# Kernel tuning notes

Measured on AMD Instinct MI355X. Metric: run time of the kernel, lower is better.

## Reference

```python
import jax, jax.numpy as jnp
import numpy as np

B, L, S, STATIC = 32, 512, 37, 8
D, DI, N, K, DTR, NL, V = 768, 1536, 16, 4, 48, 4, 32


def _rmsnorm(h, w, eps=1e-5):
    var = jnp.mean(h * h, axis=-1, keepdims=True)
    return h * jax.lax.rsqrt(var + eps) * w


def _layernorm(h, w, b, eps=1e-5):
    mu = jnp.mean(h, axis=-1, keepdims=True)
    var = jnp.mean((h - mu) ** 2, axis=-1, keepdims=True)
    return (h - mu) * jax.lax.rsqrt(var + eps) * w + b


def _selective_scan(u, dt, A, Bm, Cm):
    # u, dt: [B,L,Di]; A: [Di,N]; Bm, Cm: [B,L,N]
    def step(h, inp):
        u_t, dt_t, B_t, C_t = inp              # [B,Di],[B,Di],[B,N],[B,N]
        dA = jnp.exp(dt_t[..., None] * A)      # [B,Di,N]
        h = dA * h + (dt_t * u_t)[..., None] * B_t[:, None, :]
        y = jnp.einsum('bdn,bn->bd', h, C_t)
        return h, y
    h0 = jnp.zeros((u.shape[0], DI, N), u.dtype)
    xs = (u.transpose(1, 0, 2), dt.transpose(1, 0, 2),
          Bm.transpose(1, 0, 2), Cm.transpose(1, 0, 2))
    _, ys = jax.lax.scan(step, h0, xs)
    return ys.transpose(1, 0, 2)  # [B,L,Di]


def setup_inputs() -> dict:
    key = jax.random.key(0)
    ks = jax.random.split(key, 24)
    s = 0.02
    inp = {
        'x': jax.random.normal(ks[0], (B, L, S), jnp.float32),
        'static': jax.random.normal(ks[1], (B, STATIC), jnp.float32),
        'time': jax.random.uniform(ks[2], (B, L), jnp.float32),
        'sensor_mask': jax.random.randint(ks[3], (B, L, S), 0, 2, jnp.int32),
        'labels': jax.random.randint(ks[4], (B, L), 0, V, jnp.int64),
        # CEHR embedding params
        'emb_w': jax.random.normal(ks[5], (D, 2 * S), jnp.float32) * s,
        'emb_b': jnp.zeros((D,), jnp.float32),
        'static_w': jax.random.normal(ks[6], (D, STATIC), jnp.float32) * s,
        'static_b': jnp.zeros((D,), jnp.float32),
        'ln_w': jnp.ones((D,), jnp.float32),
        'ln_b': jnp.zeros((D,), jnp.float32),
        # Mamba layers (stacked)
        'norm_w': jnp.ones((NL, D), jnp.float32),
        'in_proj_w': jax.random.normal(ks[7], (NL, 2 * DI, D), jnp.float32) * s,
        'conv_w': jax.random.normal(ks[8], (NL, DI, K), jnp.float32) * s,
        'conv_b': jnp.zeros((NL, DI), jnp.float32),
        'x_proj_w': jax.random.normal(ks[9], (NL, DTR + 2 * N, DI), jnp.float32) * s,
        'dt_proj_w': jax.random.normal(ks[10], (NL, DI, DTR), jnp.float32) * s,
        'dt_proj_b': jnp.full((NL, DI), -4.6, jnp.float32),  # softplus^-1(~0.01)
        'A_log': jnp.broadcast_to(jnp.log(jnp.arange(1, N + 1, dtype=jnp.float32)), (NL, DI, N)).copy(),
        'D_param': jnp.ones((NL, DI), jnp.float32),
        'out_proj_w': jax.random.normal(ks[11], (NL, D, DI), jnp.float32) * s,
        'norm_f_w': jnp.ones((D,), jnp.float32),
        'lm_head_w': jax.random.normal(ks[12], (V, D), jnp.float32) * s,
    }
    return inp


def reference(x, static, time, sensor_mask, labels, emb_w, emb_b, static_w,
              static_b, ln_w, ln_b, norm_w, in_proj_w, conv_w, conv_b,
              x_proj_w, dt_proj_w, dt_proj_b, A_log, D_param, out_proj_w,
              norm_f_w, lm_head_w):
    # ---- CEHR embedding: concat(values, mask) -> D, plus static broadcast ----
    feats = jnp.concatenate([x, sensor_mask.astype(x.dtype)], axis=-1)  # [B,L,2S]
    h = jnp.einsum('blf,df->bld', feats, emb_w) + emb_b
    h = h + (static @ static_w.T + static_b)[:, None, :]
    h = _layernorm(h, ln_w, ln_b)  # [B,L,D]

    # ---- Mamba backbone ----
    for l in range(NL):
        resid = h
        hn = _rmsnorm(h, norm_w[l])
        xz = jnp.einsum('bld,ed->ble', hn, in_proj_w[l])  # [B,L,2*Di]
        xb, z = jnp.split(xz, 2, axis=-1)
        # causal depthwise conv1d, kernel K
        xp = jnp.pad(xb, ((0, 0), (K - 1, 0), (0, 0)))
        xc = sum(conv_w[l][:, k] * xp[:, k:k + L, :] for k in range(K)) + conv_b[l]
        xc = jax.nn.silu(xc)
        proj = jnp.einsum('bld,ed->ble', xc, x_proj_w[l])  # [B,L,DTR+2N]
        dt_r = proj[..., :DTR]
        Bm = proj[..., DTR:DTR + N]
        Cm = proj[..., DTR + N:]
        dt = jax.nn.softplus(jnp.einsum('blr,dr->bld', dt_r, dt_proj_w[l]) + dt_proj_b[l])
        A = -jnp.exp(A_log[l])  # [Di,N]
        y = _selective_scan(xc, dt, A, Bm, Cm) + D_param[l] * xc
        y = y * jax.nn.silu(z)
        h = resid + jnp.einsum('ble,de->bld', y, out_proj_w[l])

    h = _rmsnorm(h, norm_f_w)
    logits = jnp.einsum('bld,vd->blv', h, lm_head_w)  # [B,L,V]
    return logits
```

## Files before the change

kernel.cpp:

```cpp
#include <hip/hip_runtime.h>
#include <math.h>

#define B_ 32
#define L_ 512
#define S_ 37
#define STATIC_ 8
#define D_ 768
#define DI_ 1536
#define N_ 16
#define DTR_ 48
#define NL_ 4
#define V_ 32
#define ROWS_ (B_*L_)
#define KE_ 96
#define TCH_ 64
#define NCHT_ (L_/TCH_)
#define KS_ 4
#define KSL_ (DI_/KS_)
#define TPW_ 66
#define TPO_ 68

typedef __bf16 bf16;
typedef __bf16 bf16x8 __attribute__((ext_vector_type(8)));
typedef __bf16 bf16x4 __attribute__((ext_vector_type(4)));
typedef __bf16 bf16x2 __attribute__((ext_vector_type(2)));
typedef float f32x4 __attribute__((ext_vector_type(4)));

typedef __attribute__((address_space(3))) void lds_void;
typedef __attribute__((address_space(1))) const void gmem_void;

__device__ __forceinline__ void gld16(const void* g, void* l) {
    __builtin_amdgcn_global_load_lds((gmem_void*)g, (lds_void*)l, 16, 0, 0);
}

__device__ __forceinline__ float silu_(float x) { return x / (1.f + __expf(-x)); }
__device__ __forceinline__ float softplus_(float x) {
    return fmaxf(x, 0.f) + __logf(1.f + __expf(-fabsf(x)));
}
__device__ __forceinline__ unsigned pack_bf2_(float a, float b) {
    bf16x2 v{(bf16)a, (bf16)b};
    return __builtin_bit_cast(unsigned, v);
}
template<int CTRL>
__device__ __forceinline__ float dpp_add_(float p) {
    int vi = __builtin_amdgcn_update_dpp(0, __builtin_bit_cast(int, p),
                                         CTRL, 0xF, 0xF, true);
    return p + __builtin_bit_cast(float, vi);
}

template<int MODE>
__global__ __launch_bounds__(256) void gemm_mfma(
    const bf16* __restrict__ A, const bf16* __restrict__ W,
    const float* __restrict__ addsrc, void* __restrict__ Cv,
    int Nstore, int K, int ntn,
    const float* __restrict__ dt_bias, unsigned* __restrict__ swg,
    float* __restrict__ pbuf, const bf16* __restrict__ uref)
{
    __shared__ bf16 As[128 * 32];
    __shared__ bf16 Bs[128 * 32];
    const int tid = threadIdx.x;

    int m0, n0, kbeg, kend;
    if (MODE == 4) {
        m0 = blockIdx.y * 128; n0 = 0;
        kbeg = blockIdx.x * KSL_; kend = kbeg + KSL_;
    } else {
        int bid = blockIdx.x;
        int xcd = bid & 7, slot = bid >> 3;
        int Mtiles = gridDim.x / ntn;
        int mband = Mtiles >> 3;
        int m_tile = xcd * mband + slot / ntn;
        int n_tile = slot % ntn;
        m0 = m_tile * 128; n0 = n_tile * 128;
        kbeg = 0; kend = K;
    }

    f32x4 acc[4][4];
    #pragma unroll
    for (int i = 0; i < 4; i++)
        #pragma unroll
        for (int j = 0; j < 4; j++)
            acc[i][j] = f32x4{0.f, 0.f, 0.f, 0.f};

    const int srow = tid >> 2, spart = tid & 3;
    const bf16* ag = A + (size_t)(m0 + srow) * K + spart * 8;
    const bf16* wg = W + (size_t)(n0 + srow) * K + spart * 8;
    char* lA = (char*)As + tid * 16;
    char* lB = (char*)Bs + tid * 16;

    const int lane = tid & 63, wv = tid >> 6;
    const int wr = wv >> 1, wc = wv & 1;
    const int colL = lane & 15, quad = lane >> 4;
    const bf16* aRd = As + (wr * 64 + colL) * 32 + quad * 8;
    const bf16* bRd = Bs + (wc * 64 + colL) * 32 + quad * 8;

    for (int kt = kbeg; kt < kend; kt += 32) {
        gld16(ag + kt, lA);
        gld16(ag + kt + (size_t)64 * K, lA + 4096);
        gld16(wg + kt, lB);
        gld16(wg + kt + (size_t)64 * K, lB + 4096);
        __syncthreads();
        bf16x8 fa[4], fb[4];
        #pragma unroll
        for (int i = 0; i < 4; i++) fa[i] = *(const bf16x8*)(aRd + i * 16 * 32);
        #pragma unroll
        for (int j = 0; j < 4; j++) fb[j] = *(const bf16x8*)(bRd + j * 16 * 32);
        #pragma unroll
        for (int i = 0; i < 4; i++)
            #pragma unroll
            for (int j = 0; j < 4; j++)
                acc[i][j] = __builtin_amdgcn_mfma_f32_16x16x32_bf16(fa[i], fb[j], acc[i][j], 0, 0, 0);
        __syncthreads();
    }

    float* Cf = (float*)Cv;
    bf16*  Cb = (bf16*)Cv;
    #pragma unroll
    for (int i = 0; i < 4; i++) {
        #pragma unroll
        for (int j = 0; j < 4; j++) {
            int n = n0 + wc * 64 + j * 16 + colL;
            #pragma unroll
            for (int r = 0; r < 4; r++) {
                int m = m0 + wr * 64 + i * 16 + quad * 4 + r;
                float v = acc[i][j][r];
                if (MODE == 2) {
                    float dtv = softplus_(v + dt_bias[n]);
                    float u = (float)uref[(size_t)m * DI_ + n];
                    swg[(size_t)m * DI_ + n] = pack_bf2_(dtv * u, dtv);
                } else if (MODE == 4) {
                    if (n < 96)
                        pbuf[((size_t)blockIdx.x * Nstore + m) * 96 + n] = v;
                } else if (n < Nstore) {
                    if (addsrc) v += addsrc[(size_t)m * Nstore + n];
                    if (MODE == 1) Cb[(size_t)m * Nstore + n] = (bf16)v;
                    else           Cf[(size_t)m * Nstore + n] = v;
                }
            }
        }
    }
}

template<int MODE>
__global__ __launch_bounds__(512, 2) void gemm256(
    const bf16* __restrict__ A, const bf16* __restrict__ W,
    const float* __restrict__ addsrc, void* __restrict__ Cv,
    int Nstore, int K, int ntn)
{
    __shared__ bf16 lds[65536];
    const int tid = threadIdx.x;

    const int bid = blockIdx.x;
    const int qx = gridDim.x >> 3;
    const int wgid = (bid & 7) * qx + (bid >> 3);
    const int m0 = (wgid / ntn) * 256;
    const int n0 = (wgid % ntn) * 256;

    const int r0 = tid >> 3;
    const int scol = ((tid & 7) * 8) ^ ((r0 & 7) << 3);
    const size_t sK = (size_t)K;
    const bf16* aSrc = A + (size_t)(m0 + r0) * sK + scol;
    const bf16* bSrc = W + (size_t)(n0 + r0) * sK + scol;
    char* ldst = (char*)lds + tid * 16;

#define STAGE_A(h, t) { const bf16* s_ = aSrc + (size_t)(h) * 128 * sK + (t) * 64;   \
    char* d_ = ldst + ((t) & 1) * 65536 + (h) * 16384;                               \
    gld16(s_, d_); gld16(s_ + 64 * sK, d_ + 8192); }
#define STAGE_B(h, t) { const bf16* s_ = bSrc + (size_t)(h) * 128 * sK + (t) * 64;   \
    char* d_ = ldst + ((t) & 1) * 65536 + 32768 + (h) * 16384;                       \
    gld16(s_, d_); gld16(s_ + 64 * sK, d_ + 8192); }

    const int lane = tid & 63, w = tid >> 6;
    const int wr = w >> 2, wc = w & 3;
    const int colL = lane & 15, quad = lane >> 4;
    const int sx = (colL & 7) << 3;
    const int c0 = (quad * 8) ^ sx;
    const int c1 = c0 ^ 32;
    const bf16* aRd0 = lds + wr * 8192 + colL * 64 + c0;
    const bf16* aRd1 = lds + wr * 8192 + colL * 64 + c1;
    const bf16* bRd0 = lds + 16384 + (wc >> 1) * 8192 + ((wc & 1) * 64 + colL) * 64 + c0;
    const bf16* bRd1 = lds + 16384 + (wc >> 1) * 8192 + ((wc & 1) * 64 + colL) * 64 + c1;

    f32x4 acc[8][4];
    #pragma unroll
    for (int i = 0; i < 8; i++)
        #pragma unroll
        for (int j = 0; j < 4; j++)
            acc[i][j] = f32x4{0.f, 0.f, 0.f, 0.f};
    bf16x8 aF[4][2], bF[4][2];

#define RD_A(buf, mp) { _Pragma("unroll") for (int i = 0; i < 4; i++) {              \
    aF[i][0] = *(const bf16x8*)(aRd0 + (buf) * 32768 + (mp) * 4096 + i * 1024);      \
    aF[i][1] = *(const bf16x8*)(aRd1 + (buf) * 32768 + (mp) * 4096 + i * 1024); } }
#define RD_B01(buf) { _Pragma("unroll") for (int j = 0; j < 2; j++) {                \
    bF[j][0] = *(const bf16x8*)(bRd0 + (buf) * 32768 + j * 1024);                    \
    bF[j][1] = *(const bf16x8*)(bRd1 + (buf) * 32768 + j * 1024); } }
#define RD_B23(buf) { _Pragma("unroll") for (int j = 0; j < 2; j++) {                \
    bF[2 + j][0] = *(const bf16x8*)(bRd0 + (buf) * 32768 + (2 + j) * 1024);          \
    bF[2 + j][1] = *(const bf16x8*)(bRd1 + (buf) * 32768 + (2 + j) * 1024); } }
#define MM(mp, np) { _Pragma("unroll") for (int i = 0; i < 4; i++)                   \
    _Pragma("unroll") for (int j = 0; j < 2; j++) {                                  \
    acc[(mp)*4+i][(np)*2+j] = __builtin_amdgcn_mfma_f32_16x16x32_bf16(               \
        aF[i][0], bF[(np)*2+j][0], acc[(mp)*4+i][(np)*2+j], 0, 0, 0);                \
    acc[(mp)*4+i][(np)*2+j] = __builtin_amdgcn_mfma_f32_16x16x32_bf16(               \
        aF[i][1], bF[(np)*2+j][1], acc[(mp)*4+i][(np)*2+j], 0, 0, 0); } }
#define MID_SYNC  __builtin_amdgcn_s_barrier();                                      \
    asm volatile("s_waitcnt lgkmcnt(0)" ::: "memory");                               \
    __builtin_amdgcn_sched_barrier(0);                                               \
    __builtin_amdgcn_s_setprio(1);
#define END_PHASE __builtin_amdgcn_s_setprio(0); __builtin_amdgcn_s_barrier();

    const int NT = K >> 6;
    const int NI = NT >> 1;

    STAGE_B(0, 0); STAGE_B(1, 0); STAGE_A(0, 0); STAGE_A(1, 0);
    STAGE_B(0, 1); STAGE_B(1, 1);
    asm volatile("s_waitcnt vmcnt(4)" ::: "memory");
    __builtin_amdgcn_s_barrier();

    for (int it = 0; it < NI; ++it) {
        const int t0 = 2 * it, t1 = t0 + 1;
        const bool nlast = (it + 1 < NI);
        RD_A(0, 0); RD_B01(0);
        STAGE_A(0, t1);
        MID_SYNC; MM(0, 0); END_PHASE;
        RD_B23(0);
        STAGE_A(1, t1);
        MID_SYNC; MM(0, 1); END_PHASE;
        RD_A(0, 1);
        if (nlast) STAGE_B(0, t0 + 2);
        MID_SYNC; MM(1, 0); END_PHASE;
        if (nlast) STAGE_B(1, t0 + 2);
        MID_SYNC; MM(1, 1);
        __builtin_amdgcn_s_setprio(0);
        if (nlast) { asm volatile("s_waitcnt vmcnt(4)" ::: "memory"); }
        else       { asm volatile("s_waitcnt vmcnt(0)" ::: "memory"); }
        __builtin_amdgcn_s_barrier();
        RD_A(1, 0); RD_B01(1);
        if (nlast) STAGE_A(0, t0 + 2);
        MID_SYNC; MM(0, 0); END_PHASE;
        RD_B23(1);
        if (nlast) STAGE_A(1, t0 + 2);
        MID_SYNC; MM(0, 1); END_PHASE;
        RD_A(1, 1);
        if (nlast) STAGE_B(0, t1 + 2);
        MID_SYNC; MM(1, 0); END_PHASE;
        if (nlast) STAGE_B(1, t1 + 2);
        MID_SYNC; MM(1, 1);
        __builtin_amdgcn_s_setprio(0);
        if (nlast) { asm volatile("s_waitcnt vmcnt(4)" ::: "memory"); }
        __builtin_amdgcn_s_barrier();
    }

    float* Cf = (float*)Cv;
    bf16*  Cb = (bf16*)Cv;
    #pragma unroll
    for (int f = 0; f < 8; f++) {
        #pragma unroll
        for (int j = 0; j < 4; j++) {
            int n = n0 + wc * 64 + j * 16 + colL;
            #pragma unroll
            for (int r = 0; r < 4; r++) {
                int m = m0 + wr * 128 + f * 16 + quad * 4 + r;
                float v = acc[f][j][r];
                if (MODE == 0) {
                    v += addsrc[(size_t)m * Nstore + n];
                    Cf[(size_t)m * Nstore + n] = v;
                } else {
                    Cb[(size_t)m * Nstore + n] = (bf16)v;
                }
            }
        }
    }
#undef STAGE_A
#undef STAGE_B
#undef RD_A
#undef RD_B01
#undef RD_B23
#undef MM
#undef MID_SYNC
#undef END_PHASE
}

__global__ __launch_bounds__(256) void xpost_kernel(const float* __restrict__ pbuf,
                                                    bf16* __restrict__ dtr,
                                                    float* __restrict__ bcf,
                                                    int crows) {
    int idx = blockIdx.x * 256 + threadIdx.x;
    int m = idx / 96, j = idx % 96;
    float s = pbuf[idx];
    #pragma unroll
    for (int k = 1; k < KS_; k++) s += pbuf[(size_t)k * crows * 96 + idx];
    if (j < 64) {
        dtr[(size_t)m * 64 + j] = (bf16)s;
    } else {
        int jj = j - 64;
        int n = jj & 15, hi = jj >> 4;
        int bb = m >> 9, t = m & 511;
        int ct = t >> 6, tl = t & 63;
        int byo = (n * 512 + tl * 8 + hi * 4) ^ ((n & 7) << 4);
        *(float*)((char*)bcf + (size_t)(bb * 8 + ct) * 8192 + byo) = s;
    }
}

__global__ __launch_bounds__(256) void cast_f2b_kernel(const float* __restrict__ s,
                                                       bf16* __restrict__ d) {
    size_t i = (size_t)blockIdx.x * 256 + threadIdx.x;
    d[i] = (bf16)s[i];
}

__global__ __launch_bounds__(256) void pad_lm_kernel(const float* __restrict__ s, bf16* __restrict__ d) {
    int i = blockIdx.x * 256 + threadIdx.x;
    int row = i / D_;
    d[i] = (row < V_) ? (bf16)s[i] : (bf16)0.f;
}

__global__ __launch_bounds__(256) void pad_embw_kernel(const float* __restrict__ s, bf16* __restrict__ d) {
    int i = blockIdx.x * 256 + threadIdx.x;
    int row = i / KE_, col = i % KE_;
    d[i] = (col < 2 * S_) ? (bf16)s[row * 2 * S_ + col] : (bf16)0.f;
}

__global__ __launch_bounds__(256) void feats_kernel(const float* __restrict__ x,
                                                    const int* __restrict__ mask,
                                                    bf16* __restrict__ d) {
    size_t i = (size_t)blockIdx.x * 256 + threadIdx.x;
    size_t row = i / KE_;
    int col = (int)(i % KE_);
    float v = 0.f;
    if (col < S_) v = x[row * S_ + col];
    else if (col < 2 * S_) v = (float)mask[row * S_ + (col - S_)];
    d[i] = (bf16)v;
}

__global__ __launch_bounds__(256) void xpw_pad_kernel(const float* __restrict__ xpw,
                                                      bf16* __restrict__ d) {
    int l = blockIdx.y;
    int idx = blockIdx.x * 256 + threadIdx.x;
    int row = idx / DI_, col = idx % DI_;
    float v = 0.f;
    if (row < DTR_) v = xpw[((size_t)l * (DTR_ + 2 * N_) + row) * DI_ + col];
    else if (row >= 64 && row < 96) v = xpw[((size_t)l * (DTR_ + 2 * N_) + row - 16) * DI_ + col];
    d[(size_t)l * 128 * DI_ + idx] = (bf16)v;
}

__global__ __launch_bounds__(256) void dtw_pad_kernel(const float* __restrict__ dtw,
                                                      bf16* __restrict__ d) {
    int l = blockIdx.y;
    int idx = blockIdx.x * 256 + threadIdx.x;
    int row = idx / 64, c = idx % 64;
    float v = (c < DTR_) ? dtw[((size_t)l * DI_ + row) * DTR_ + c] : 0.f;
    d[(size_t)l * DI_ * 64 + idx] = (bf16)v;
}

__global__ __launch_bounds__(256) void sstat_kernel(const float* __restrict__ stat,
                                                    const float* __restrict__ static_w,
                                                    const float* __restrict__ static_b,
                                                    const float* __restrict__ emb_b,
                                                    float* __restrict__ sstat) {
    int i = blockIdx.x * 256 + threadIdx.x;
    int d = i % D_, b = i / D_;
    float acc = emb_b[d] + static_b[d];
    const float* sw = static_w + (size_t)d * STATIC_;
    const float* sv = stat + (size_t)b * STATIC_;
    #pragma unroll
    for (int s = 0; s < STATIC_; s++) acc += sv[s] * sw[s];
    sstat[i] = acc;
}

__device__ __forceinline__ void block_reduce2_(float& a, float& b, float* sbuf) {
    #pragma unroll
    for (int off = 32; off > 0; off >>= 1) {
        a += __shfl_down(a, off, 64);
        b += __shfl_down(b, off, 64);
    }
    int lane = threadIdx.x & 63, wid = threadIdx.x >> 6;
    if (lane == 0) { sbuf[wid] = a; sbuf[4 + wid] = b; }
    __syncthreads();
    a = sbuf[0] + sbuf[1] + sbuf[2] + sbuf[3];
    b = sbuf[4] + sbuf[5] + sbuf[6] + sbuf[7];
}

__global__ __launch_bounds__(256) void ln_embed_kernel(const float* __restrict__ h_pre,
                                                       const float* __restrict__ sstat,
                                                       const float* __restrict__ ln_w,
                                                       const float* __restrict__ ln_b,
                                                       float* __restrict__ h) {
    int row = blockIdx.x, b = row / L_, tid = threadIdx.x;
    __shared__ float sbuf[8];
    float v[3], sum = 0.f, sq = 0.f;
    #pragma unroll
    for (int j = 0; j < 3; j++) {
        int d = tid + 256 * j;
        v[j] = h_pre[(size_t)row * D_ + d] + sstat[b * D_ + d];
        sum += v[j]; sq += v[j] * v[j];
    }
    block_reduce2_(sum, sq, sbuf);
    float mu = sum * (1.f / D_);
    float rstd = rsqrtf(sq * (1.f / D_) - mu * mu + 1e-5f);
    #pragma unroll
    for (int j = 0; j < 3; j++) {
        int d = tid + 256 * j;
        h[(size_t)row * D_ + d] = (v[j] - mu) * rstd * ln_w[d] + ln_b[d];
    }
}

__global__ __launch_bounds__(256) void rmsnorm_bf_kernel(const float* __restrict__ h,
                                                         const float* __restrict__ w,
                                                         bf16* __restrict__ out) {
    int row = blockIdx.x, tid = threadIdx.x;
    __shared__ float sbuf[8];
    float v[3], ss = 0.f, dummy = 0.f;
    #pragma unroll
    for (int j = 0; j < 3; j++) {
        v[j] = h[(size_t)row * D_ + tid + 256 * j];
        ss += v[j] * v[j];
    }
    block_reduce2_(ss, dummy, sbuf);
    float rstd = rsqrtf(ss * (1.f / D_) + 1e-5f);
    #pragma unroll
    for (int j = 0; j < 3; j++) {
        int d = tid + 256 * j;
        out[(size_t)row * D_ + d] = (bf16)(v[j] * rstd * w[d]);
    }
}

__global__ __launch_bounds__(256) void conv_silu_kernel(const bf16* __restrict__ xzb,
                                                        const float* __restrict__ cw,
                                                        const float* __restrict__ cb,
                                                        const float* __restrict__ Dp,
                                                        bf16* __restrict__ xcb,
                                                        unsigned* __restrict__ gag) {
    size_t idx = (size_t)blockIdx.x * 256 + threadIdx.x;
    int d4 = (int)(idx % (DI_ / 4));
    size_t row = idx / (DI_ / 4);
    int t = (int)(row % L_);
    int d = d4 * 4;
    const uint2* xz64 = (const uint2*)xzb;
    size_t base = row * 768 + d4;
    uint2 z2{0u, 0u};
    uint2 p0  = xz64[base];
    uint2 pm1 = (t >= 1) ? xz64[base - 768]     : z2;
    uint2 pm2 = (t >= 2) ? xz64[base - 2 * 768] : z2;
    uint2 pm3 = (t >= 3) ? xz64[base - 3 * 768] : z2;
    uint2 pz  = xz64[base + 384];

    bf16x4 a0 = __builtin_bit_cast(bf16x4, p0);
    bf16x4 a1 = __builtin_bit_cast(bf16x4, pm1);
    bf16x4 a2 = __builtin_bit_cast(bf16x4, pm2);
    bf16x4 a3 = __builtin_bit_cast(bf16x4, pm3);
    bf16x4 az = __builtin_bit_cast(bf16x4, pz);

    float cbl[4], Dl[4];
    *(float4*)cbl = ((const float4*)cb)[d4];
    *(float4*)Dl  = ((const float4*)Dp)[d4];

    float u[4];
    unsigned gv[4];
    #pragma unroll
    for (int c = 0; c < 4; c++) {
        float4 wc = ((const float4*)cw)[d + c];
        float acc = cbl[c] + wc.x * (float)a3[c] + wc.y * (float)a2[c]
                           + wc.z * (float)a1[c] + wc.w * (float)a0[c];
        u[c] = silu_(acc);
        float gz = silu_((float)az[c]);
        gv[c] = pack_bf2_(Dl[c] * u[c] * gz, gz);
    }
    ((uint2*)xcb)[row * (DI_ / 4) + d4] = uint2{pack_bf2_(u[0], u[1]), pack_bf2_(u[2], u[3])};
    *(uint4*)(gag + row * DI_ + d) = uint4{gv[0], gv[1], gv[2], gv[3]};
}

__global__ __launch_bounds__(256) void scan_lds_kernel(const float* __restrict__ bcf,
                                                       const unsigned* __restrict__ swg,
                                                       const unsigned* __restrict__ gag,
                                                       const float* __restrict__ A_log,
                                                       bf16* __restrict__ yb) {
    __shared__ float2   lsw2[16][TPW_];
    __shared__ char     lbcf[2][8192];
    __shared__ unsigned logds[16][TPO_];
    const int tid = threadIdx.x;
    const int n = tid & 15, dl = tid >> 4;
    const int d0 = blockIdx.x * 16;
    const int d = d0 + dl;
    const int b = blockIdx.y;
    const float AvL = -__expf(A_log[(size_t)d * N_ + n]) * 1.44269504f;
    const size_t seqbase = (size_t)b * L_;

    const char* bcf_base = (const char*)bcf + (size_t)b * NCHT_ * 8192;
    unsigned swr[4], gar[4];

    #define BCF_GLD(c) { const char* s_ = bcf_base + (size_t)(c) * 8192 + tid * 16;  \
        char* d_ = (char*)lbcf + ((c) & 1) * 8192 + tid * 16;                        \
        gld16(s_, d_); gld16(s_ + 4096, d_ + 4096); }
    #define REG_LOAD(c) { size_t rb = seqbase + (size_t)(c) * TCH_;                  \
        _Pragma("unroll") for (int i = 0; i < 4; i++) {                              \
            size_t g = (rb + dl + 16 * i) * DI_ + d0 + n;                            \
            swr[i] = swg[g]; gar[i] = gag[g]; } }
    #define DSWRITE() { _Pragma("unroll") for (int i = 0; i < 4; i++) {              \
            int t = dl + 16 * i;                                                     \
            bf16x2 w2 = __builtin_bit_cast(bf16x2, swr[i]);                          \
            lsw2[n][t] = float2{(float)w2.x, (float)w2.y};                           \
            logds[n][t] = gar[i]; } }

    BCF_GLD(0);
    REG_LOAD(0);
    DSWRITE();
    __syncthreads();
    REG_LOAD(1);

    float h = 0.f;
    for (int c = 0; c < NCHT_; c++) {
        if (c + 1 < NCHT_) BCF_GLD(c + 1);
        bf16* pyc = yb + (seqbase + (size_t)c * TCH_) * DI_ + d;
        const char* bcrow = (const char*)lbcf + (c & 1) * 8192;
        #pragma unroll
        for (int tb = 0; tb < TCH_; tb += 16) {
            float res = 0.f;
            #pragma unroll
            for (int tq = 0; tq < 16; tq += 2) {
                float4 dd = *(const float4*)&lsw2[dl][tb + tq];
                int byo = (n * 512 + (tb + tq) * 8) ^ ((n & 7) << 4);
                float4 bc = *(const float4*)(bcrow + byo);
                #pragma unroll
                for (int u = 0; u < 2; u++) {
                    float du  = u ? dd.z : dd.x;
                    float dtv = u ? dd.w : dd.y;
                    float Bv  = u ? bc.z : bc.x;
                    float Cv  = u ? bc.w : bc.y;
                    float dA = __builtin_amdgcn_exp2f(dtv * AvL);
                    h = dA * h + du * Bv;
                    float pq = h * Cv;
                    pq = dpp_add_<0xB1>(pq);
                    pq = dpp_add_<0x4E>(pq);
                    pq = dpp_add_<0x124>(pq);
                    pq = dpp_add_<0x128>(pq);
                    if (n == tq + u) res = pq;
                }
            }
            unsigned og = logds[dl][tb + n];
            bf16x2 o2 = __builtin_bit_cast(bf16x2, og);
            pyc[(size_t)(tb + n) * DI_] = (bf16)(res * (float)o2.y + (float)o2.x);
        }
        if (c + 1 < NCHT_) {
            __syncthreads();
            DSWRITE();
            __syncthreads();
            if (c + 2 < NCHT_) REG_LOAD(c + 2);
        }
    }
    #undef BCF_GLD
    #undef REG_LOAD
    #undef DSWRITE
}

extern "C" void kernel_launch(void* const* d_in, const int* in_sizes, int n_in,
                              void* d_out, int out_size, void* d_ws, size_t ws_size,
                              hipStream_t stream) {
    const float* x        = (const float*)d_in[0];
    const float* stat     = (const float*)d_in[1];
    const int*   mask     = (const int*)d_in[3];
    const float* emb_w    = (const float*)d_in[5];
    const float* emb_b    = (const float*)d_in[6];
    const float* static_w = (const float*)d_in[7];
    const float* static_b = (const float*)d_in[8];
    const float* ln_w     = (const float*)d_in[9];
    const float* ln_b     = (const float*)d_in[10];
    const float* norm_w   = (const float*)d_in[11];
    const float* in_proj_w  = (const float*)d_in[12];
    const float* conv_w   = (const float*)d_in[13];
    const float* conv_b   = (const float*)d_in[14];
    const float* x_proj_w = (const float*)d_in[15];
    const float* dt_proj_w= (const float*)d_in[16];
    const float* dt_proj_b= (const float*)d_in[17];
    const float* A_log    = (const float*)d_in[18];
    const float* D_param  = (const float*)d_in[19];
    const float* out_proj_w = (const float*)d_in[20];
    const float* norm_f_w = (const float*)d_in[21];
    const float* lm_head_w= (const float*)d_in[22];
    float* out = (float*)d_out;

    const int CBr = 8;
    const int CROWSr = CBr * L_;
    const int NCHr = B_ / CBr;

    char* p = (char*)d_ws;
    float*    h      = (float*)p;         p += (size_t)ROWS_ * D_ * 4;
    bf16*     hn_bf  = (bf16*)p;          p += (size_t)CROWSr * D_ * 2;
    char*     xz_region = p;
    bf16*     xz_bf  = (bf16*)p;          p += (size_t)CROWSr * 2 * DI_ * 2;
    bf16*     xc_bf  = (bf16*)p;          p += (size_t)CROWSr * DI_ * 2;
    unsigned* sw_g   = (unsigned*)p;      p += (size_t)CROWSr * DI_ * 4;
    unsigned* gate_g = (unsigned*)p;      p += (size_t)CROWSr * DI_ * 4;
    float*    bcf    = (float*)p;         p += (size_t)CROWSr * 32 * 4;
    bf16*     dtr_bf = (bf16*)p;          p += (size_t)CROWSr * 64 * 2;
    float*    pbuf   = (float*)p;         p += (size_t)KS_ * CROWSr * 96 * 4;
    bf16*     y_bf   = (bf16*)p;          p += (size_t)ROWS_ * DI_ * 2;
    bf16*     inw_l  = (bf16*)p;          p += (size_t)2 * DI_ * D_ * 2;
    bf16*     outw_l = (bf16*)p;          p += (size_t)D_ * DI_ * 2;
    bf16*     xpwp_bf= (bf16*)p;          p += (size_t)NL_ * 128 * DI_ * 2;
    bf16*     dtwp_bf= (bf16*)p;          p += (size_t)NL_ * DI_ * 64 * 2;
    bf16*     lmw_bf = (bf16*)p;          p += (size_t)128 * D_ * 2;
    bf16*     embw_bf= (bf16*)p;          p += (size_t)D_ * KE_ * 2;
    bf16*     feats  = (bf16*)p;          p += (size_t)ROWS_ * KE_ * 2;
    float*    sstat  = (float*)p;         p += (size_t)B_ * D_ * 4;
    float*    h_pre  = (float*)xz_region;
    bf16*     hn_full= (bf16*)sw_g;

    pad_lm_kernel<<<(128 * D_) / 256, 256, 0, stream>>>(lm_head_w, lmw_bf);
    pad_embw_kernel<<<(D_ * KE_) / 256, 256, 0, stream>>>(emb_w, embw_bf);
    feats_kernel<<<(ROWS_ * KE_) / 256, 256, 0, stream>>>(x, mask, feats);
    dim3 gxp((128 * DI_) / 256, NL_);
    xpw_pad_kernel<<<gxp, 256, 0, stream>>>(x_proj_w, xpwp_bf);
    dim3 gdt((DI_ * 64) / 256, NL_);
    dtw_pad_kernel<<<gdt, 256, 0, stream>>>(dt_proj_w, dtwp_bf);
    sstat_kernel<<<(B_ * D_) / 256, 256, 0, stream>>>(stat, static_w, static_b, emb_b, sstat);

    gemm_mfma<0><<<(D_ / 128) * (ROWS_ / 128), 256, 0, stream>>>(
        feats, embw_bf, nullptr, h_pre, D_, KE_, D_ / 128,
        nullptr, nullptr, nullptr, nullptr);
    ln_embed_kernel<<<ROWS_, 256, 0, stream>>>(h_pre, sstat, ln_w, ln_b, h);

    for (int l = 0; l < NL_; l++) {
        cast_f2b_kernel<<<(2 * DI_ * D_) / 256, 256, 0, stream>>>(
            in_proj_w + (size_t)l * 2 * DI_ * D_, inw_l);
        cast_f2b_kernel<<<(D_ * DI_) / 256, 256, 0, stream>>>(
            out_proj_w + (size_t)l * D_ * DI_, outw_l);

        for (int c = 0; c < NCHr; c++) {
            float* hc = h + (size_t)c * CROWSr * D_;

            rmsnorm_bf_kernel<<<CROWSr, 256, 0, stream>>>(hc, norm_w + (size_t)l * D_, hn_bf);

            gemm256<1><<<(CROWSr / 256) * (2 * DI_ / 256), 512, 0, stream>>>(
                hn_bf, inw_l, nullptr, xz_bf, 2 * DI_, D_, 2 * DI_ / 256);

            conv_silu_kernel<<<(CROWSr * (DI_ / 4)) / 256, 256, 0, stream>>>(
                xz_bf, conv_w + (size_t)l * DI_ * 4, conv_b + (size_t)l * DI_,
                D_param + (size_t)l * DI_, xc_bf, gate_g);

            dim3 g2a(KS_, CROWSr / 128);
            gemm_mfma<4><<<g2a, 256, 0, stream>>>(xc_bf, xpwp_bf + (size_t)l * 128 * DI_,
                                                  nullptr, nullptr, CROWSr, DI_, 1,
                                                  nullptr, nullptr, pbuf, nullptr);
            xpost_kernel<<<(CROWSr * 96) / 256, 256, 0, stream>>>(pbuf, dtr_bf, bcf, CROWSr);

            gemm_mfma<2><<<(DI_ / 128) * (CROWSr / 128), 256, 0, stream>>>(
                dtr_bf, dtwp_bf + (size_t)l * DI_ * 64, nullptr, nullptr, 0, 64, DI_ / 128,
                dt_proj_b + (size_t)l * DI_, sw_g, nullptr, xc_bf);

            dim3 gs(DI_ / 16, CBr);
            scan_lds_kernel<<<gs, 256, 0, stream>>>(bcf, sw_g, gate_g,
                                                    A_log + (size_t)l * DI_ * N_,
                                                    y_bf + (size_t)c * CROWSr * DI_);
        }

        gemm256<0><<<(ROWS_ / 256) * (D_ / 256), 512, 0, stream>>>(
            y_bf, outw_l, h, h, D_, DI_, D_ / 256);
    }

    rmsnorm_bf_kernel<<<ROWS_, 256, 0, stream>>>(h, norm_f_w, hn_full);
    gemm_mfma<0><<<ROWS_ / 128, 256, 0, stream>>>(
        hn_full, lmw_bf, nullptr, out, V_, D_, 1,
        nullptr, nullptr, nullptr, nullptr);
}
```

Baseline: 2.412 ms.

## Give each scan thread four state lanes and relayout B/C buffer by time

Each thread in the selective scan now keeps four of the sixteen state dimensions, so one channel needs four lanes instead of sixteen. This cuts the cross-lane reduction from four DPP steps to two and spreads the exp and FMA work over fewer threads. The B/C staging buffer is changed from an n-major swizzled layout to a time-major one so each lane reads its four (B,C) pairs with two vector loads. Blocks shrink to 128 threads covering 32 channels, and each thread now holds sixteen staged values per array in registers, which raises register use and lowers thread-level parallelism per channel.

Result: slower. 2.754 ms (+14.2%).

```diff
diff --git a/kernel.cpp b/kernel.cpp
--- a/kernel.cpp
+++ b/kernel.cpp
@@ -17,8 +17,6 @@
 #define NCHT_ (L_/TCH_)
 #define KS_ 4
 #define KSL_ (DI_/KS_)
-#define TPW_ 66
-#define TPO_ 68
 
 typedef __bf16 bf16;
 typedef __bf16 bf16x8 __attribute__((ext_vector_type(8)));
@@ -298,7 +296,7 @@
         int n = jj & 15, hi = jj >> 4;
         int bb = m >> 9, t = m & 511;
         int ct = t >> 6, tl = t & 63;
-        int byo = (n * 512 + tl * 8 + hi * 4) ^ ((n & 7) << 4);
+        int byo = tl * 128 + (n >> 2) * 32 + (n & 3) * 8 + hi * 4;
         *(float*)((char*)bcf + (size_t)(bb * 8 + ct) * 8192 + byo) = s;
     }
 }
@@ -470,37 +468,50 @@
     *(uint4*)(gag + row * DI_ + d) = uint4{gv[0], gv[1], gv[2], gv[3]};
 }
 
-__global__ __launch_bounds__(256) void scan_lds_kernel(const float* __restrict__ bcf,
+__global__ __launch_bounds__(128) void scan_lds_kernel(const float* __restrict__ bcf,
                                                        const unsigned* __restrict__ swg,
                                                        const unsigned* __restrict__ gag,
                                                        const float* __restrict__ A_log,
                                                        bf16* __restrict__ yb) {
-    __shared__ float2   lsw2[16][TPW_];
+    __shared__ float2   lsw2[TCH_][32];
+    __shared__ unsigned logds[TCH_][36];
     __shared__ char     lbcf[2][8192];
-    __shared__ unsigned logds[16][TPO_];
     const int tid = threadIdx.x;
-    const int n = tid & 15, dl = tid >> 4;
-    const int d0 = blockIdx.x * 16;
-    const int d = d0 + dl;
+    const int q = tid & 3;
+    const int bd = (tid >> 2) & 31;
+    const int w = tid >> 6;
+    const int dl = (tid & 63) >> 2;
+    const int bdd = w * 16 + dl;
+    const int d0blk = blockIdx.x * 32;
+    const int d = d0blk + bdd;
     const int b = blockIdx.y;
-    const float AvL = -__expf(A_log[(size_t)d * N_ + n]) * 1.44269504f;
     const size_t seqbase = (size_t)b * L_;
 
+    f32x4 av = *(const f32x4*)(A_log + (size_t)d * N_ + q * 4);
+    float AvL0 = -__expf(av[0]) * 1.44269504f;
+    float AvL1 = -__expf(av[1]) * 1.44269504f;
+    float AvL2 = -__expf(av[2]) * 1.44269504f;
+    float AvL3 = -__expf(av[3]) * 1.44269504f;
+
     const char* bcf_base = (const char*)bcf + (size_t)b * NCHT_ * 8192;
-    unsigned swr[4], gar[4];
+    unsigned swr[16], gar[16];
 
     #define BCF_GLD(c) { const char* s_ = bcf_base + (size_t)(c) * 8192 + tid * 16;  \
         char* d_ = (char*)lbcf + ((c) & 1) * 8192 + tid * 16;                        \
-        gld16(s_, d_); gld16(s_ + 4096, d_ + 4096); }
-    #define REG_LOAD(c) { size_t rb = seqbase + (size_t)(c) * TCH_;                  \
-        _Pragma("unroll") for (int i = 0; i < 4; i++) {                              \
-            size_t g = (rb + dl + 16 * i) * DI_ + d0 + n;                            \
+        gld16(s_, d_); gld16(s_ + 2048, d_ + 2048);                                  \
+        gld16(s_ + 4096, d_ + 4096); gld16(s_ + 6144, d_ + 6144); }
+    #define REG_LOAD(c) { size_t rb = seqbase + (size_t)(c) * TCH_ + (tid >> 5) * 16;\
+        int dd_ = tid & 31;                                                          \
+        _Pragma("unroll")                                                            \
+        for (int i = 0; i < 16; i++) {                                               \
+            size_t g = (rb + i) * DI_ + d0blk + dd_;                                 \
             swr[i] = swg[g]; gar[i] = gag[g]; } }
-    #define DSWRITE() { _Pragma("unroll") for (int i = 0; i < 4; i++) {              \
-            int t = dl + 16 * i;                                                     \
+    #define DSWRITE() { int tt_ = (tid >> 5) * 16; int dd_ = tid & 31;               \
+        _Pragma("unroll")                                                            \
+        for (int i = 0; i < 16; i++) {                                               \
             bf16x2 w2 = __builtin_bit_cast(bf16x2, swr[i]);                          \
-            lsw2[n][t] = float2{(float)w2.x, (float)w2.y};                           \
-            logds[n][t] = gar[i]; } }
+            lsw2[tt_ + i][dd_] = float2{(float)w2.x, (float)w2.y};                   \
+            logds[tt_ + i][dd_] = gar[i]; } }
 
     BCF_GLD(0);
     REG_LOAD(0);
@@ -508,38 +519,36 @@
     __syncthreads();
     REG_LOAD(1);
 
-    float h = 0.f;
+    float h0 = 0.f, h1 = 0.f, h2 = 0.f, h3 = 0.f;
     for (int c = 0; c < NCHT_; c++) {
         if (c + 1 < NCHT_) BCF_GLD(c + 1);
         bf16* pyc = yb + (seqbase + (size_t)c * TCH_) * DI_ + d;
         const char* bcrow = (const char*)lbcf + (c & 1) * 8192;
         #pragma unroll
-        for (int tb = 0; tb < TCH_; tb += 16) {
+        for (int tb = 0; tb < TCH_; tb += 4) {
             float res = 0.f;
             #pragma unroll
-            for (int tq = 0; tq < 16; tq += 2) {
-                float4 dd = *(const float4*)&lsw2[dl][tb + tq];
-                int byo = (n * 512 + (tb + tq) * 8) ^ ((n & 7) << 4);
-                float4 bc = *(const float4*)(bcrow + byo);
-                #pragma unroll
-                for (int u = 0; u < 2; u++) {
-                    float du  = u ? dd.z : dd.x;
-                    float dtv = u ? dd.w : dd.y;
-                    float Bv  = u ? bc.z : bc.x;
-                    float Cv  = u ? bc.w : bc.y;
-                    float dA = __builtin_amdgcn_exp2f(dtv * AvL);
-                    h = dA * h + du * Bv;
-                    float pq = h * Cv;
-                    pq = dpp_add_<0xB1>(pq);
-                    pq = dpp_add_<0x4E>(pq);
-                    pq = dpp_add_<0x124>(pq);
-                    pq = dpp_add_<0x128>(pq);
-                    if (n == tq + u) res = pq;
-                }
+            for (int u = 0; u < 4; u++) {
+                const int t = tb + u;
+                float2 dd2 = lsw2[t][bdd];
+                f32x4 bcA = *(const f32x4*)(bcrow + t * 128 + q * 32);
+                f32x4 bcB = *(const f32x4*)(bcrow + t * 128 + q * 32 + 16);
+                float du = dd2.x, dtv = dd2.y;
+                h0 = __builtin_amdgcn_exp2f(dtv * AvL0) * h0 + du * bcA[0];
+                float p = h0 * bcA[1];
+                h1 = __builtin_amdgcn_exp2f(dtv * AvL1) * h1 + du * bcA[2];
+                p += h1 * bcA[3];
+                h2 = __builtin_amdgcn_exp2f(dtv * AvL2) * h2 + du * bcB[0];
+                p += h2 * bcB[1];
+                h3 = __builtin_amdgcn_exp2f(dtv * AvL3) * h3 + du * bcB[2];
+                p += h3 * bcB[3];
+                p = dpp_add_<0xB1>(p);
+                p = dpp_add_<0x4E>(p);
+                if (q == u) res = p;
             }
-            unsigned og = logds[dl][tb + n];
+            unsigned og = logds[tb + q][bdd];
             bf16x2 o2 = __builtin_bit_cast(bf16x2, og);
-            pyc[(size_t)(tb + n) * DI_] = (bf16)(res * (float)o2.y + (float)o2.x);
+            pyc[(size_t)(tb + q) * DI_] = (bf16)(res * (float)o2.y + (float)o2.x);
         }
         if (c + 1 < NCHT_) {
             __syncthreads();
@@ -648,8 +657,8 @@
                 dtr_bf, dtwp_bf + (size_t)l * DI_ * 64, nullptr, nullptr, 0, 64, DI_ / 128,
                 dt_proj_b + (size_t)l * DI_, sw_g, nullptr, xc_bf);
 
-            dim3 gs(DI_ / 16, CBr);
-            scan_lds_kernel<<<gs, 256, 0, stream>>>(bcf, sw_g, gate_g,
+            dim3 gs(DI_ / 32, CBr);
+            scan_lds_kernel<<<gs, 128, 0, stream>>>(bcf, sw_g, gate_g,
                                                     A_log + (size_t)l * DI_ * N_,
                                                     y_bf + (size_t)c * CROWSr * DI_);
         }
```
